# Performance work log

Measured on AMD Instinct MI355X. Metric: run time of the kernel, lower is better.

Reference implementation:

```python
import jax, jax.numpy as jnp
import numpy as np

B, L, C_IN = 16, 512, 32
D_MODEL, D_STATE, D_CONV, EXPAND, PRED_LEN = 128, 16, 4, 2, 96
D_INNER = EXPAND * D_MODEL          # 256
DT_RANK = (D_MODEL + 15) // 16      # 8 (ceil(d_model/16), mamba_ssm default)


def setup_inputs() -> dict:
    key = jax.random.key(0)
    ks = jax.random.split(key, 14)
    f32 = jnp.float32
    nrm = lambda k, shape, sc: jax.random.normal(k, shape, f32) * sc
    inp = {
        "x": jax.random.normal(ks[0], (B, L, C_IN), f32),
        # input_proj: Linear(enc_in, d_model)
        "W_in": nrm(ks[1], (C_IN, D_MODEL), C_IN ** -0.5),
        "b_in": jnp.zeros((D_MODEL,), f32),
        # Mamba in_proj: Linear(d_model, 2*d_inner, bias=False)
        "W_inproj": nrm(ks[2], (D_MODEL, 2 * D_INNER), D_MODEL ** -0.5),
        # depthwise causal conv1d (d_inner, d_conv) + bias
        "conv_w": nrm(ks[3], (D_INNER, D_CONV), D_CONV ** -0.5),
        "conv_b": jnp.zeros((D_INNER,), f32),
        # x_proj: Linear(d_inner, dt_rank + 2*d_state, bias=False)
        "W_xproj": nrm(ks[4], (D_INNER, DT_RANK + 2 * D_STATE), D_INNER ** -0.5),
        # dt_proj: Linear(dt_rank, d_inner) with bias init so softplus(bias) ~ 1e-3..1e-1
        "W_dt": nrm(ks[5], (DT_RANK, D_INNER), DT_RANK ** -0.5),
        "b_dt": jax.random.uniform(ks[6], (D_INNER,), f32, minval=-6.0, maxval=-3.0),
        # S4D-real A init: A = -exp(A_log), A_log = log(1..d_state)
        "A_log": jnp.log(jnp.tile(jnp.arange(1, D_STATE + 1, dtype=f32), (D_INNER, 1))),
        "D": jnp.ones((D_INNER,), f32),
        # Mamba out_proj: Linear(d_inner, d_model, bias=False)
        "W_out": nrm(ks[7], (D_INNER, D_MODEL), D_INNER ** -0.5),
        # output_proj: Linear(d_model*seq_len, pred_len*enc_in)
        "W_outproj": nrm(ks[8], (D_MODEL * L, PRED_LEN * C_IN), (D_MODEL * L) ** -0.5),
        "b_outproj": jnp.zeros((PRED_LEN * C_IN,), f32),
    }
    return inp


def _mamba_forward(x, W_in, b_in, W_inproj, conv_w, conv_b, W_xproj,
                   W_dt, b_dt, A_log, D, W_out, W_outproj, b_outproj):
    Bb, Ll, Cc = x.shape
    d_inner, d_conv = conv_w.shape
    d_state = A_log.shape[1]
    dt_rank = W_dt.shape[0]

    h = x @ W_in + b_in                                  # (B,L,d_model)
    xz = h @ W_inproj                                    # (B,L,2*d_inner)
    u, z = jnp.split(xz, 2, axis=-1)                     # each (B,L,d_inner)

    # causal depthwise conv1d along L
    uc = jnp.transpose(u, (0, 2, 1))                     # (B,d_inner,L)
    kern = conv_w[:, None, :]                            # (d_inner,1,d_conv)
    uc = jax.lax.conv_general_dilated(
        uc, kern, window_strides=(1,), padding=[(d_conv - 1, 0)],
        dimension_numbers=("NCH", "OIH", "NCH"), feature_group_count=d_inner)
    u = jax.nn.silu(jnp.transpose(uc, (0, 2, 1)) + conv_b)   # (B,L,d_inner)

    # input-dependent dt, B, C
    xdbc = u @ W_xproj                                   # (B,L,dt_rank+2*d_state)
    dt = jax.nn.softplus(xdbc[..., :dt_rank] @ W_dt + b_dt)  # (B,L,d_inner)
    Bm = xdbc[..., dt_rank:dt_rank + d_state]            # (B,L,d_state)
    Cm = xdbc[..., dt_rank + d_state:]                   # (B,L,d_state)

    A = -jnp.exp(A_log)                                  # (d_inner,d_state)
    dA = jnp.exp(jnp.einsum('bld,dn->bldn', dt, A))      # discretized A
    dBu = jnp.einsum('bld,bln,bld->bldn', dt, Bm, u)     # discretized B*u

    def step(hstate, inputs):
        dA_t, dBu_t, C_t = inputs                        # (B,d,n),(B,d,n),(B,n)
        hstate = dA_t * hstate + dBu_t
        y_t = jnp.einsum('bdn,bn->bd', hstate, C_t)
        return hstate, y_t

    h0 = jnp.zeros((Bb, d_inner, d_state), u.dtype)
    _, ys = jax.lax.scan(step, h0, (jnp.moveaxis(dA, 1, 0),
                                    jnp.moveaxis(dBu, 1, 0),
                                    jnp.moveaxis(Cm, 1, 0)))
    y = jnp.moveaxis(ys, 0, 1) + u * D                   # (B,L,d_inner)
    y = y * jax.nn.silu(z)                               # gating
    m_out = y @ W_out                                    # (B,L,d_model)

    flat = m_out.reshape(Bb, -1)                         # (B, L*d_model)
    pred = flat @ W_outproj + b_outproj                  # (B, pred_len*enc_in)
    return pred.reshape(Bb, W_outproj.shape[1] // Cc, Cc)


def reference(x, W_in, b_in, W_inproj, conv_w, conv_b, W_xproj,
              W_dt, b_dt, A_log, D, W_out, W_outproj, b_outproj):
    return _mamba_forward(x, W_in, b_in, W_inproj, conv_w, conv_b, W_xproj,
                          W_dt, b_dt, A_log, D, W_out, W_outproj, b_outproj)
```

## Files before the change

### kernel.cpp

```cpp
#include <hip/hip_runtime.h>
#include <math.h>

#define NB 16
#define LL 512
#define CIN 32
#define DM 128
#define DS 16
#define DI 256
#define DTR 8
#define NCOL 3072
#define KTOT 65536
#define ROWS 8192
#define CH 64
#define CLEN 8
#define KC 512
#define KS 128
#define OUTSZ 49152

typedef float f32x2 __attribute__((ext_vector_type(2)));

__device__ __forceinline__ float sigmoidf_(float x){ return 1.f/(1.f+expf(-x)); }
__device__ __forceinline__ float softplusf_(float x){ return (x > 20.f) ? x : log1pf(expf(x)); }

__global__ void __launch_bounds__(256) k_A(
    const float* __restrict__ x, const float* __restrict__ W_in,
    const float* __restrict__ b_in, const float* __restrict__ W_ip,
    const float* __restrict__ cw, const float* __restrict__ cb,
    float* __restrict__ u, float* __restrict__ z) {
  __shared__ float xs[11][32];
  __shared__ float hs[11][128];
  __shared__ float up[11][256];
  int t = threadIdx.x;
  int b  = blockIdx.x >> 6;
  int lt = blockIdx.x & 63;
  int l0 = lt * 8;
  for (int i=t; i<11*32; i+=256) {
    int r = i >> 5, c = i & 31;
    int li = l0 - 3 + r;
    xs[r][c] = (li >= 0) ? x[((b<<9)+li)*CIN + c] : 0.f;
  }
  __syncthreads();
  for (int i=t; i<11*128; i+=256) {
    int r = i >> 7, c = i & 127;
    float acc = b_in[c];
    #pragma unroll
    for (int k=0;k<CIN;k++) acc = fmaf(xs[r][k], W_in[k*DM+c], acc);
    hs[r][c] = acc;
  }
  __syncthreads();
  {
    int c0 = (t & 63)*4;
    int r0 = (t >> 6)*3;
    bool has2 = (r0+2 < 11);
    float acc[3][4] = {};
    for (int k4=0;k4<32;k4++) {
      float4 h0v = *(const float4*)&hs[r0][k4*4];
      float4 h1v = *(const float4*)&hs[r0+1][k4*4];
      float4 h2v = has2 ? *(const float4*)&hs[r0+2][k4*4] : make_float4(0.f,0.f,0.f,0.f);
      float h0a[4]={h0v.x,h0v.y,h0v.z,h0v.w};
      float h1a[4]={h1v.x,h1v.y,h1v.z,h1v.w};
      float h2a[4]={h2v.x,h2v.y,h2v.z,h2v.w};
      #pragma unroll
      for (int j=0;j<4;j++) {
        float4 w = *(const float4*)(W_ip + (k4*4+j)*512 + c0);
        acc[0][0]=fmaf(h0a[j],w.x,acc[0][0]); acc[0][1]=fmaf(h0a[j],w.y,acc[0][1]);
        acc[0][2]=fmaf(h0a[j],w.z,acc[0][2]); acc[0][3]=fmaf(h0a[j],w.w,acc[0][3]);
        acc[1][0]=fmaf(h1a[j],w.x,acc[1][0]); acc[1][1]=fmaf(h1a[j],w.y,acc[1][1]);
        acc[1][2]=fmaf(h1a[j],w.z,acc[1][2]); acc[1][3]=fmaf(h1a[j],w.w,acc[1][3]);
        acc[2][0]=fmaf(h2a[j],w.x,acc[2][0]); acc[2][1]=fmaf(h2a[j],w.y,acc[2][1]);
        acc[2][2]=fmaf(h2a[j],w.z,acc[2][2]); acc[2][3]=fmaf(h2a[j],w.w,acc[2][3]);
      }
    }
    *(float4*)&up[r0  ][c0] = make_float4(acc[0][0],acc[0][1],acc[0][2],acc[0][3]);
    *(float4*)&up[r0+1][c0] = make_float4(acc[1][0],acc[1][1],acc[1][2],acc[1][3]);
    if (has2)
      *(float4*)&up[r0+2][c0] = make_float4(acc[2][0],acc[2][1],acc[2][2],acc[2][3]);
  }
  {
    int c0 = (t & 63)*4;
    int r0 = (t >> 6)*2;
    float acc[2][4] = {};
    for (int k4=0;k4<32;k4++) {
      float4 h0v = *(const float4*)&hs[3+r0][k4*4];
      float4 h1v = *(const float4*)&hs[3+r0+1][k4*4];
      float h0a[4]={h0v.x,h0v.y,h0v.z,h0v.w};
      float h1a[4]={h1v.x,h1v.y,h1v.z,h1v.w};
      #pragma unroll
      for (int j=0;j<4;j++) {
        float4 w = *(const float4*)(W_ip + (k4*4+j)*512 + 256 + c0);
        acc[0][0]=fmaf(h0a[j],w.x,acc[0][0]); acc[0][1]=fmaf(h0a[j],w.y,acc[0][1]);
        acc[0][2]=fmaf(h0a[j],w.z,acc[0][2]); acc[0][3]=fmaf(h0a[j],w.w,acc[0][3]);
        acc[1][0]=fmaf(h1a[j],w.x,acc[1][0]); acc[1][1]=fmaf(h1a[j],w.y,acc[1][1]);
        acc[1][2]=fmaf(h1a[j],w.z,acc[1][2]); acc[1][3]=fmaf(h1a[j],w.w,acc[1][3]);
      }
    }
    #pragma unroll
    for (int i=0;i<2;i++) {
      int gr = (b<<9) + l0 + r0 + i;
      *(float4*)(z + gr*DI + c0) =
        make_float4(acc[i][0],acc[i][1],acc[i][2],acc[i][3]);
    }
  }
  __syncthreads();
  for (int i=t; i<8*256; i+=256) {
    int r = i >> 8, d = i & 255;
    float s = cb[d];
    #pragma unroll
    for (int j=0;j<4;j++) {
      int li = l0 + r - 3 + j;
      if (li >= 0) s = fmaf(cw[d*4+j], up[r+j][d], s);
    }
    int gr = (b<<9) + l0 + r;
    u[gr*DI + d] = s * sigmoidf_(s);
  }
}

__global__ void __launch_bounds__(256) k_xproj(
    const float* __restrict__ u, const float* __restrict__ W_xp,
    float* __restrict__ xdbc) {
  __shared__ float Wt[40][260];
  int t = threadIdx.x;
  for (int i=t; i<256*40; i+=256) {
    int k = i / 40, c = i - k*40;
    Wt[c][k] = W_xp[i];
  }
  __syncthreads();
  int idx = blockIdx.x*256 + t;
  int r = idx / 40, c = idx - r*40;
  const float4* ur4 = (const float4*)(u + r*DI);
  const float4* wc4 = (const float4*)&Wt[c][0];
  float acc = 0.f;
  #pragma unroll 8
  for (int k4=0;k4<64;k4++) {
    float4 uv = ur4[k4];
    float4 wv = wc4[k4];
    acc = fmaf(uv.x, wv.x, acc);
    acc = fmaf(uv.y, wv.y, acc);
    acc = fmaf(uv.z, wv.z, acc);
    acc = fmaf(uv.w, wv.w, acc);
  }
  xdbc[idx] = acc;
}

__global__ void __launch_bounds__(256) k_scan1(
    const float* __restrict__ u, const float* __restrict__ xdbc,
    const float* __restrict__ Wdt, const float* __restrict__ bdt,
    const float* __restrict__ A_log,
    float* __restrict__ Hc, float* __restrict__ Sdt) {
  __shared__ float xl[CLEN][40];
  int t = threadIdx.x;
  int b = blockIdx.x >> 6, c = blockIdx.x & 63, d = t;
  int l0 = c * CLEN;
  int row0 = (b<<9) + l0;
  for (int i=t; i<CLEN*40; i+=256) xl[i/40][i%40] = xdbc[row0*40 + i];
  __syncthreads();
  float A[16], hsv[16];
  #pragma unroll
  for (int n=0;n<16;n++){ A[n] = -expf(A_log[d*16+n]); hsv[n]=0.f; }
  float wdt[DTR];
  #pragma unroll
  for (int j=0;j<DTR;j++) wdt[j] = Wdt[j*DI+d];
  float bdtv = bdt[d];
  float sdt = 0.f;
  for (int l=0;l<CLEN;++l) {
    float acc = bdtv;
    #pragma unroll
    for (int j=0;j<DTR;j++) acc = fmaf(xl[l][j], wdt[j], acc);
    float dtv = softplusf_(acc);
    sdt += dtv;
    float du = dtv * u[((row0+l)<<8) + d];
    #pragma unroll
    for (int n=0;n<16;n++) {
      float a = expf(dtv*A[n]);
      hsv[n] = fmaf(a, hsv[n], du * xl[l][DTR+n]);
    }
  }
  int bd = (b<<8) + d;
  int base = (bd*CH + c)*16;
  #pragma unroll
  for (int n=0;n<16;n++) Hc[base+n] = hsv[n];
  Sdt[bd*CH + c] = sdt;
}

__global__ void k_scan2(const float* __restrict__ A_log, const float* __restrict__ Hc,
                        const float* __restrict__ Sdt, float* __restrict__ Hst) {
  int idx = blockIdx.x*256 + threadIdx.x;
  int n  = idx & 15;
  int bd = idx >> 4;
  int d  = bd & 255;
  float A = -expf(A_log[d*16+n]);
  float hs = 0.f;
  int base = bd*CH*16;
  for (int c=0;c<CH;c++) {
    Hst[base + c*16 + n] = hs;
    float sdt = Sdt[bd*CH + c];
    hs = fmaf(expf(A*sdt), hs, Hc[base + c*16 + n]);
  }
}

__global__ void __launch_bounds__(256) k_scan3(
    const float* __restrict__ u, const float* __restrict__ z,
    const float* __restrict__ xdbc, const float* __restrict__ Wdt,
    const float* __restrict__ bdt, const float* __restrict__ A_log,
    const float* __restrict__ Dp, const float* __restrict__ Hst,
    const float* __restrict__ W_out, float* __restrict__ mo) {
  __shared__ float ym[CLEN][256];
  __shared__ float xl[CLEN][40];
  int t = threadIdx.x;
  int b = blockIdx.x >> 6, c = blockIdx.x & 63, d = t;
  int l0 = c * CLEN;
  int row0 = (b<<9) + l0;
  for (int i=t; i<CLEN*40; i+=256) xl[i/40][i%40] = xdbc[row0*40 + i];
  __syncthreads();
  int bd = (b<<8) + d;
  int base = (bd*CH + c)*16;
  float A[16], hsv[16];
  #pragma unroll
  for (int n=0;n<16;n++){ A[n] = -expf(A_log[d*16+n]); hsv[n] = Hst[base+n]; }
  float wdt[DTR];
  #pragma unroll
  for (int j=0;j<DTR;j++) wdt[j] = Wdt[j*DI+d];
  float bdtv = bdt[d];
  float Dv = Dp[d];
  for (int l=0;l<CLEN;++l) {
    int row = row0 + l;
    float acc = bdtv;
    #pragma unroll
    for (int j=0;j<DTR;j++) acc = fmaf(xl[l][j], wdt[j], acc);
    float dtv = softplusf_(acc);
    float uv = u[(row<<8) + d];
    float zv = z[(row<<8) + d];
    float du = dtv * uv;
    float y = 0.f;
    #pragma unroll
    for (int n=0;n<16;n++) {
      float a = expf(dtv*A[n]);
      hsv[n] = fmaf(a, hsv[n], du * xl[l][DTR+n]);
      y = fmaf(hsv[n], xl[l][DTR+DS+n], y);
    }
    y = fmaf(uv, Dv, y);
    ym[l][d] = y * (zv * sigmoidf_(zv));
  }
  __syncthreads();
  int cc = t & 127;
  int rg = (t >> 7) * 4;
  float acc[4] = {};
  for (int k4=0;k4<64;k4++) {
    float w0 = W_out[(k4*4+0)*DM+cc];
    float w1 = W_out[(k4*4+1)*DM+cc];
    float w2 = W_out[(k4*4+2)*DM+cc];
    float w3 = W_out[(k4*4+3)*DM+cc];
    #pragma unroll
    for (int o=0;o<4;o++) {
      float4 yv = *(const float4*)&ym[rg+o][k4*4];
      acc[o] = fmaf(yv.w, w3, fmaf(yv.z, w2, fmaf(yv.y, w1, fmaf(yv.x, w0, acc[o]))));
    }
  }
  #pragma unroll
  for (int o=0;o<4;o++) mo[(row0+rg+o)*DM + cc] = acc[o];
}

__global__ void __launch_bounds__(256) k_final(
    const float* __restrict__ flat, const float* __restrict__ W,
    float* __restrict__ part) {
  __shared__ float lds[KC][16];
  int t = threadIdx.x;
  int n0 = blockIdx.x * 512;
  int k0 = blockIdx.y * KC;
  for (int i = t; i < 16*(KC/4); i += 256) {
    int bb  = i & 15;
    int kk4 = i >> 4;
    float4 v = *(const float4*)(flat + bb*KTOT + k0 + kk4*4);
    lds[kk4*4+0][bb] = v.x; lds[kk4*4+1][bb] = v.y;
    lds[kk4*4+2][bb] = v.z; lds[kk4*4+3][bb] = v.w;
  }
  __syncthreads();
  int c0 = n0 + t*2;
  float2 acc[16];
  #pragma unroll
  for (int b=0;b<16;b++) acc[b] = make_float2(0.f,0.f);
  const float* Wp = W + (size_t)k0*NCOL + c0;
  for (int kk=0; kk<KC; kk+=4) {
    f32x2 w0 = __builtin_nontemporal_load((const f32x2*)(Wp + (size_t)(kk+0)*NCOL));
    f32x2 w1 = __builtin_nontemporal_load((const f32x2*)(Wp + (size_t)(kk+1)*NCOL));
    f32x2 w2 = __builtin_nontemporal_load((const f32x2*)(Wp + (size_t)(kk+2)*NCOL));
    f32x2 w3 = __builtin_nontemporal_load((const f32x2*)(Wp + (size_t)(kk+3)*NCOL));
    const float4* f0 = (const float4*)&lds[kk+0][0];
    const float4* f1 = (const float4*)&lds[kk+1][0];
    const float4* f2 = (const float4*)&lds[kk+2][0];
    const float4* f3 = (const float4*)&lds[kk+3][0];
    #pragma unroll
    for (int q=0;q<4;q++) {
      float4 fa = f0[q], fb = f1[q], fc = f2[q], fd = f3[q];
      float fs0[4] = {fa.x,fa.y,fa.z,fa.w};
      float fs1[4] = {fb.x,fb.y,fb.z,fb.w};
      float fs2[4] = {fc.x,fc.y,fc.z,fc.w};
      float fs3[4] = {fd.x,fd.y,fd.z,fd.w};
      #pragma unroll
      for (int j=0;j<4;j++) {
        int b = q*4+j;
        acc[b].x=fmaf(fs0[j],w0.x,acc[b].x); acc[b].y=fmaf(fs0[j],w0.y,acc[b].y);
        acc[b].x=fmaf(fs1[j],w1.x,acc[b].x); acc[b].y=fmaf(fs1[j],w1.y,acc[b].y);
        acc[b].x=fmaf(fs2[j],w2.x,acc[b].x); acc[b].y=fmaf(fs2[j],w2.y,acc[b].y);
        acc[b].x=fmaf(fs3[j],w3.x,acc[b].x); acc[b].y=fmaf(fs3[j],w3.y,acc[b].y);
      }
    }
  }
  float* p = part + (size_t)blockIdx.y*OUTSZ;
  #pragma unroll
  for (int b=0;b<16;b++) {
    f32x2 v; v.x = acc[b].x; v.y = acc[b].y;
    __builtin_nontemporal_store(v, (f32x2*)(p + b*NCOL + c0));
  }
}

__global__ void k_reduce(const float* __restrict__ part, const float* __restrict__ bias,
                         float* __restrict__ out) {
  int idx = blockIdx.x*256 + threadIdx.x;
  float acc = bias[idx % NCOL];
  #pragma unroll 8
  for (int s=0;s<KS;s++)
    acc += __builtin_nontemporal_load(part + (size_t)s*OUTSZ + idx);
  out[idx] = acc;
}

extern "C" void kernel_launch(void* const* d_in, const int* in_sizes, int n_in,
                              void* d_out, int out_size, void* d_ws, size_t ws_size,
                              hipStream_t stream) {
  const float* x        = (const float*)d_in[0];
  const float* W_in     = (const float*)d_in[1];
  const float* b_in     = (const float*)d_in[2];
  const float* W_inproj = (const float*)d_in[3];
  const float* conv_w   = (const float*)d_in[4];
  const float* conv_b   = (const float*)d_in[5];
  const float* W_xproj  = (const float*)d_in[6];
  const float* W_dt     = (const float*)d_in[7];
  const float* b_dt     = (const float*)d_in[8];
  const float* A_log    = (const float*)d_in[9];
  const float* Dp       = (const float*)d_in[10];
  const float* W_out    = (const float*)d_in[11];
  const float* W_outproj= (const float*)d_in[12];
  const float* b_outproj= (const float*)d_in[13];
  float* out = (float*)d_out;
  float* ws  = (float*)d_ws;

  float* u    = ws;
  float* z    = ws + 2097152;
  float* xdbc = ws + 4194304;
  float* Hc   = ws + 4521984;
  float* Sdt  = ws + 8716288;
  float* Hst  = ws + 8978432;
  float* mo   = ws + 13172736;
  float* part = ws + 14221312;

  k_A     <<<1024, 256, 0, stream>>>(x, W_in, b_in, W_inproj, conv_w, conv_b, u, z);
  k_xproj <<<1280, 256, 0, stream>>>(u, W_xproj, xdbc);
  k_scan1 <<<1024, 256, 0, stream>>>(u, xdbc, W_dt, b_dt, A_log, Hc, Sdt);
  k_scan2 <<<256,  256, 0, stream>>>(A_log, Hc, Sdt, Hst);
  k_scan3 <<<1024, 256, 0, stream>>>(u, z, xdbc, W_dt, b_dt, A_log, Dp, Hst, W_out, mo);
  k_final <<<dim3(6, KS), 256, 0, stream>>>(mo, W_outproj, part);
  k_reduce<<<192,  256, 0, stream>>>(part, b_outproj, out);
}
```

Measured before the change: 290.4 us.

## Merge five pre-projection kernels into one cooperative kernel with grid syncs

Replaces the separate input-projection, x_proj, chunk-scan, chunk-carry and output-scan kernels with a single cooperative kernel of 512 blocks. The stages are separated by grid.sync(), and each block loops over two work units per stage. This removes four kernel launch boundaries. The x_proj stage also drops its LDS-transposed weight staging and reads W_xproj directly from global memory. In exchange, the kernel has higher LDS usage, half-idle grid phases (the carry stage uses only 256 blocks), grid-barrier costs, and uncoalesced weight reads in x_proj.

```diff
diff --git a/kernel.cpp b/kernel.cpp
--- a/kernel.cpp
+++ b/kernel.cpp
@@ -1,5 +1,8 @@
 #include <hip/hip_runtime.h>
+#include <hip/hip_cooperative_groups.h>
 #include <math.h>
+
+namespace cg = cooperative_groups;
 
 #define NB 16
 #define LL 512
@@ -16,248 +19,243 @@
 #define KC 512
 #define KS 128
 #define OUTSZ 49152
+#define MGRID 512
 
 typedef float f32x2 __attribute__((ext_vector_type(2)));
 
 __device__ __forceinline__ float sigmoidf_(float x){ return 1.f/(1.f+expf(-x)); }
 __device__ __forceinline__ float softplusf_(float x){ return (x > 20.f) ? x : log1pf(expf(x)); }
 
-__global__ void __launch_bounds__(256) k_A(
+__global__ void __launch_bounds__(256) k_mega(
     const float* __restrict__ x, const float* __restrict__ W_in,
     const float* __restrict__ b_in, const float* __restrict__ W_ip,
     const float* __restrict__ cw, const float* __restrict__ cb,
-    float* __restrict__ u, float* __restrict__ z) {
+    const float* __restrict__ W_xp, const float* __restrict__ Wdt,
+    const float* __restrict__ bdt, const float* __restrict__ A_log,
+    const float* __restrict__ Dp, const float* __restrict__ W_out,
+    float* __restrict__ u, float* __restrict__ z,
+    float* __restrict__ xdbc, float* __restrict__ Hc,
+    float* __restrict__ Sdt, float* __restrict__ Hst,
+    float* __restrict__ mo) {
+  cg::grid_group grid = cg::this_grid();
   __shared__ float xs[11][32];
   __shared__ float hs[11][128];
   __shared__ float up[11][256];
+  __shared__ float xl[CLEN][40];
+  __shared__ float ym[CLEN][256];
   int t = threadIdx.x;
-  int b  = blockIdx.x >> 6;
-  int lt = blockIdx.x & 63;
-  int l0 = lt * 8;
-  for (int i=t; i<11*32; i+=256) {
-    int r = i >> 5, c = i & 31;
-    int li = l0 - 3 + r;
-    xs[r][c] = (li >= 0) ? x[((b<<9)+li)*CIN + c] : 0.f;
-  }
-  __syncthreads();
-  for (int i=t; i<11*128; i+=256) {
-    int r = i >> 7, c = i & 127;
-    float acc = b_in[c];
-    #pragma unroll
-    for (int k=0;k<CIN;k++) acc = fmaf(xs[r][k], W_in[k*DM+c], acc);
-    hs[r][c] = acc;
-  }
-  __syncthreads();
-  {
-    int c0 = (t & 63)*4;
-    int r0 = (t >> 6)*3;
-    bool has2 = (r0+2 < 11);
-    float acc[3][4] = {};
-    for (int k4=0;k4<32;k4++) {
-      float4 h0v = *(const float4*)&hs[r0][k4*4];
-      float4 h1v = *(const float4*)&hs[r0+1][k4*4];
-      float4 h2v = has2 ? *(const float4*)&hs[r0+2][k4*4] : make_float4(0.f,0.f,0.f,0.f);
-      float h0a[4]={h0v.x,h0v.y,h0v.z,h0v.w};
-      float h1a[4]={h1v.x,h1v.y,h1v.z,h1v.w};
-      float h2a[4]={h2v.x,h2v.y,h2v.z,h2v.w};
+
+  for (int rep=0; rep<2; ++rep) {
+    int unit = blockIdx.x + (rep<<9);
+    int b = unit >> 6;
+    int l0 = (unit & 63) * 8;
+    for (int i=t; i<11*32; i+=256) {
+      int r = i >> 5, c = i & 31;
+      int li = l0 - 3 + r;
+      xs[r][c] = (li >= 0) ? x[((b<<9)+li)*CIN + c] : 0.f;
+    }
+    __syncthreads();
+    for (int i=t; i<11*128; i+=256) {
+      int r = i >> 7, c = i & 127;
+      float acc = b_in[c];
+      #pragma unroll
+      for (int k=0;k<CIN;k++) acc = fmaf(xs[r][k], W_in[k*DM+c], acc);
+      hs[r][c] = acc;
+    }
+    __syncthreads();
+    {
+      int c0 = (t & 63)*4;
+      int r0 = (t >> 6)*3;
+      bool has2 = (r0+2 < 11);
+      float acc[3][4] = {};
+      for (int k4=0;k4<32;k4++) {
+        float4 h0v = *(const float4*)&hs[r0][k4*4];
+        float4 h1v = *(const float4*)&hs[r0+1][k4*4];
+        float4 h2v = has2 ? *(const float4*)&hs[r0+2][k4*4] : make_float4(0.f,0.f,0.f,0.f);
+        float h0a[4]={h0v.x,h0v.y,h0v.z,h0v.w};
+        float h1a[4]={h1v.x,h1v.y,h1v.z,h1v.w};
+        float h2a[4]={h2v.x,h2v.y,h2v.z,h2v.w};
+        #pragma unroll
+        for (int j=0;j<4;j++) {
+          float4 w = *(const float4*)(W_ip + (k4*4+j)*512 + c0);
+          acc[0][0]=fmaf(h0a[j],w.x,acc[0][0]); acc[0][1]=fmaf(h0a[j],w.y,acc[0][1]);
+          acc[0][2]=fmaf(h0a[j],w.z,acc[0][2]); acc[0][3]=fmaf(h0a[j],w.w,acc[0][3]);
+          acc[1][0]=fmaf(h1a[j],w.x,acc[1][0]); acc[1][1]=fmaf(h1a[j],w.y,acc[1][1]);
+          acc[1][2]=fmaf(h1a[j],w.z,acc[1][2]); acc[1][3]=fmaf(h1a[j],w.w,acc[1][3]);
+          acc[2][0]=fmaf(h2a[j],w.x,acc[2][0]); acc[2][1]=fmaf(h2a[j],w.y,acc[2][1]);
+          acc[2][2]=fmaf(h2a[j],w.z,acc[2][2]); acc[2][3]=fmaf(h2a[j],w.w,acc[2][3]);
+        }
+      }
+      *(float4*)&up[r0  ][c0] = make_float4(acc[0][0],acc[0][1],acc[0][2],acc[0][3]);
+      *(float4*)&up[r0+1][c0] = make_float4(acc[1][0],acc[1][1],acc[1][2],acc[1][3]);
+      if (has2)
+        *(float4*)&up[r0+2][c0] = make_float4(acc[2][0],acc[2][1],acc[2][2],acc[2][3]);
+    }
+    {
+      int c0 = (t & 63)*4;
+      int r0 = (t >> 6)*2;
+      float acc[2][4] = {};
+      for (int k4=0;k4<32;k4++) {
+        float4 h0v = *(const float4*)&hs[3+r0][k4*4];
+        float4 h1v = *(const float4*)&hs[3+r0+1][k4*4];
+        float h0a[4]={h0v.x,h0v.y,h0v.z,h0v.w};
+        float h1a[4]={h1v.x,h1v.y,h1v.z,h1v.w};
+        #pragma unroll
+        for (int j=0;j<4;j++) {
+          float4 w = *(const float4*)(W_ip + (k4*4+j)*512 + 256 + c0);
+          acc[0][0]=fmaf(h0a[j],w.x,acc[0][0]); acc[0][1]=fmaf(h0a[j],w.y,acc[0][1]);
+          acc[0][2]=fmaf(h0a[j],w.z,acc[0][2]); acc[0][3]=fmaf(h0a[j],w.w,acc[0][3]);
+          acc[1][0]=fmaf(h1a[j],w.x,acc[1][0]); acc[1][1]=fmaf(h1a[j],w.y,acc[1][1]);
+          acc[1][2]=fmaf(h1a[j],w.z,acc[1][2]); acc[1][3]=fmaf(h1a[j],w.w,acc[1][3]);
+        }
+      }
+      #pragma unroll
+      for (int i=0;i<2;i++) {
+        int gr = (b<<9) + l0 + r0 + i;
+        *(float4*)(z + gr*DI + c0) =
+          make_float4(acc[i][0],acc[i][1],acc[i][2],acc[i][3]);
+      }
+    }
+    __syncthreads();
+    for (int i=t; i<8*256; i+=256) {
+      int r = i >> 8, d = i & 255;
+      float s = cb[d];
       #pragma unroll
       for (int j=0;j<4;j++) {
-        float4 w = *(const float4*)(W_ip + (k4*4+j)*512 + c0);
-        acc[0][0]=fmaf(h0a[j],w.x,acc[0][0]); acc[0][1]=fmaf(h0a[j],w.y,acc[0][1]);
-        acc[0][2]=fmaf(h0a[j],w.z,acc[0][2]); acc[0][3]=fmaf(h0a[j],w.w,acc[0][3]);
-        acc[1][0]=fmaf(h1a[j],w.x,acc[1][0]); acc[1][1]=fmaf(h1a[j],w.y,acc[1][1]);
-        acc[1][2]=fmaf(h1a[j],w.z,acc[1][2]); acc[1][3]=fmaf(h1a[j],w.w,acc[1][3]);
-        acc[2][0]=fmaf(h2a[j],w.x,acc[2][0]); acc[2][1]=fmaf(h2a[j],w.y,acc[2][1]);
-        acc[2][2]=fmaf(h2a[j],w.z,acc[2][2]); acc[2][3]=fmaf(h2a[j],w.w,acc[2][3]);
-      }
-    }
-    *(float4*)&up[r0  ][c0] = make_float4(acc[0][0],acc[0][1],acc[0][2],acc[0][3]);
-    *(float4*)&up[r0+1][c0] = make_float4(acc[1][0],acc[1][1],acc[1][2],acc[1][3]);
-    if (has2)
-      *(float4*)&up[r0+2][c0] = make_float4(acc[2][0],acc[2][1],acc[2][2],acc[2][3]);
-  }
-  {
-    int c0 = (t & 63)*4;
-    int r0 = (t >> 6)*2;
-    float acc[2][4] = {};
-    for (int k4=0;k4<32;k4++) {
-      float4 h0v = *(const float4*)&hs[3+r0][k4*4];
-      float4 h1v = *(const float4*)&hs[3+r0+1][k4*4];
-      float h0a[4]={h0v.x,h0v.y,h0v.z,h0v.w};
-      float h1a[4]={h1v.x,h1v.y,h1v.z,h1v.w};
-      #pragma unroll
-      for (int j=0;j<4;j++) {
-        float4 w = *(const float4*)(W_ip + (k4*4+j)*512 + 256 + c0);
-        acc[0][0]=fmaf(h0a[j],w.x,acc[0][0]); acc[0][1]=fmaf(h0a[j],w.y,acc[0][1]);
-        acc[0][2]=fmaf(h0a[j],w.z,acc[0][2]); acc[0][3]=fmaf(h0a[j],w.w,acc[0][3]);
-        acc[1][0]=fmaf(h1a[j],w.x,acc[1][0]); acc[1][1]=fmaf(h1a[j],w.y,acc[1][1]);
-        acc[1][2]=fmaf(h1a[j],w.z,acc[1][2]); acc[1][3]=fmaf(h1a[j],w.w,acc[1][3]);
-      }
-    }
-    #pragma unroll
-    for (int i=0;i<2;i++) {
-      int gr = (b<<9) + l0 + r0 + i;
-      *(float4*)(z + gr*DI + c0) =
-        make_float4(acc[i][0],acc[i][1],acc[i][2],acc[i][3]);
-    }
-  }
-  __syncthreads();
-  for (int i=t; i<8*256; i+=256) {
-    int r = i >> 8, d = i & 255;
-    float s = cb[d];
-    #pragma unroll
-    for (int j=0;j<4;j++) {
-      int li = l0 + r - 3 + j;
-      if (li >= 0) s = fmaf(cw[d*4+j], up[r+j][d], s);
-    }
-    int gr = (b<<9) + l0 + r;
-    u[gr*DI + d] = s * sigmoidf_(s);
-  }
-}
-
-__global__ void __launch_bounds__(256) k_xproj(
-    const float* __restrict__ u, const float* __restrict__ W_xp,
-    float* __restrict__ xdbc) {
-  __shared__ float Wt[40][260];
-  int t = threadIdx.x;
-  for (int i=t; i<256*40; i+=256) {
-    int k = i / 40, c = i - k*40;
-    Wt[c][k] = W_xp[i];
-  }
-  __syncthreads();
-  int idx = blockIdx.x*256 + t;
-  int r = idx / 40, c = idx - r*40;
-  const float4* ur4 = (const float4*)(u + r*DI);
-  const float4* wc4 = (const float4*)&Wt[c][0];
-  float acc = 0.f;
-  #pragma unroll 8
-  for (int k4=0;k4<64;k4++) {
-    float4 uv = ur4[k4];
-    float4 wv = wc4[k4];
-    acc = fmaf(uv.x, wv.x, acc);
-    acc = fmaf(uv.y, wv.y, acc);
-    acc = fmaf(uv.z, wv.z, acc);
-    acc = fmaf(uv.w, wv.w, acc);
-  }
-  xdbc[idx] = acc;
-}
-
-__global__ void __launch_bounds__(256) k_scan1(
-    const float* __restrict__ u, const float* __restrict__ xdbc,
-    const float* __restrict__ Wdt, const float* __restrict__ bdt,
-    const float* __restrict__ A_log,
-    float* __restrict__ Hc, float* __restrict__ Sdt) {
-  __shared__ float xl[CLEN][40];
-  int t = threadIdx.x;
-  int b = blockIdx.x >> 6, c = blockIdx.x & 63, d = t;
-  int l0 = c * CLEN;
-  int row0 = (b<<9) + l0;
-  for (int i=t; i<CLEN*40; i+=256) xl[i/40][i%40] = xdbc[row0*40 + i];
-  __syncthreads();
-  float A[16], hsv[16];
-  #pragma unroll
-  for (int n=0;n<16;n++){ A[n] = -expf(A_log[d*16+n]); hsv[n]=0.f; }
-  float wdt[DTR];
-  #pragma unroll
-  for (int j=0;j<DTR;j++) wdt[j] = Wdt[j*DI+d];
-  float bdtv = bdt[d];
-  float sdt = 0.f;
-  for (int l=0;l<CLEN;++l) {
-    float acc = bdtv;
-    #pragma unroll
-    for (int j=0;j<DTR;j++) acc = fmaf(xl[l][j], wdt[j], acc);
-    float dtv = softplusf_(acc);
-    sdt += dtv;
-    float du = dtv * u[((row0+l)<<8) + d];
-    #pragma unroll
-    for (int n=0;n<16;n++) {
-      float a = expf(dtv*A[n]);
-      hsv[n] = fmaf(a, hsv[n], du * xl[l][DTR+n]);
-    }
-  }
-  int bd = (b<<8) + d;
-  int base = (bd*CH + c)*16;
-  #pragma unroll
-  for (int n=0;n<16;n++) Hc[base+n] = hsv[n];
-  Sdt[bd*CH + c] = sdt;
-}
-
-__global__ void k_scan2(const float* __restrict__ A_log, const float* __restrict__ Hc,
-                        const float* __restrict__ Sdt, float* __restrict__ Hst) {
-  int idx = blockIdx.x*256 + threadIdx.x;
-  int n  = idx & 15;
-  int bd = idx >> 4;
-  int d  = bd & 255;
-  float A = -expf(A_log[d*16+n]);
-  float hs = 0.f;
-  int base = bd*CH*16;
-  for (int c=0;c<CH;c++) {
-    Hst[base + c*16 + n] = hs;
-    float sdt = Sdt[bd*CH + c];
-    hs = fmaf(expf(A*sdt), hs, Hc[base + c*16 + n]);
-  }
-}
-
-__global__ void __launch_bounds__(256) k_scan3(
-    const float* __restrict__ u, const float* __restrict__ z,
-    const float* __restrict__ xdbc, const float* __restrict__ Wdt,
-    const float* __restrict__ bdt, const float* __restrict__ A_log,
-    const float* __restrict__ Dp, const float* __restrict__ Hst,
-    const float* __restrict__ W_out, float* __restrict__ mo) {
-  __shared__ float ym[CLEN][256];
-  __shared__ float xl[CLEN][40];
-  int t = threadIdx.x;
-  int b = blockIdx.x >> 6, c = blockIdx.x & 63, d = t;
-  int l0 = c * CLEN;
-  int row0 = (b<<9) + l0;
-  for (int i=t; i<CLEN*40; i+=256) xl[i/40][i%40] = xdbc[row0*40 + i];
-  __syncthreads();
-  int bd = (b<<8) + d;
-  int base = (bd*CH + c)*16;
-  float A[16], hsv[16];
-  #pragma unroll
-  for (int n=0;n<16;n++){ A[n] = -expf(A_log[d*16+n]); hsv[n] = Hst[base+n]; }
-  float wdt[DTR];
-  #pragma unroll
-  for (int j=0;j<DTR;j++) wdt[j] = Wdt[j*DI+d];
-  float bdtv = bdt[d];
-  float Dv = Dp[d];
-  for (int l=0;l<CLEN;++l) {
-    int row = row0 + l;
-    float acc = bdtv;
-    #pragma unroll
-    for (int j=0;j<DTR;j++) acc = fmaf(xl[l][j], wdt[j], acc);
-    float dtv = softplusf_(acc);
-    float uv = u[(row<<8) + d];
-    float zv = z[(row<<8) + d];
-    float du = dtv * uv;
-    float y = 0.f;
-    #pragma unroll
-    for (int n=0;n<16;n++) {
-      float a = expf(dtv*A[n]);
-      hsv[n] = fmaf(a, hsv[n], du * xl[l][DTR+n]);
-      y = fmaf(hsv[n], xl[l][DTR+DS+n], y);
-    }
-    y = fmaf(uv, Dv, y);
-    ym[l][d] = y * (zv * sigmoidf_(zv));
-  }
-  __syncthreads();
-  int cc = t & 127;
-  int rg = (t >> 7) * 4;
-  float acc[4] = {};
-  for (int k4=0;k4<64;k4++) {
-    float w0 = W_out[(k4*4+0)*DM+cc];
-    float w1 = W_out[(k4*4+1)*DM+cc];
-    float w2 = W_out[(k4*4+2)*DM+cc];
-    float w3 = W_out[(k4*4+3)*DM+cc];
-    #pragma unroll
-    for (int o=0;o<4;o++) {
-      float4 yv = *(const float4*)&ym[rg+o][k4*4];
-      acc[o] = fmaf(yv.w, w3, fmaf(yv.z, w2, fmaf(yv.y, w1, fmaf(yv.x, w0, acc[o]))));
-    }
-  }
-  #pragma unroll
-  for (int o=0;o<4;o++) mo[(row0+rg+o)*DM + cc] = acc[o];
+        int li = l0 + r - 3 + j;
+        if (li >= 0) s = fmaf(cw[d*4+j], up[r+j][d], s);
+      }
+      int gr = (b<<9) + l0 + r;
+      u[gr*DI + d] = s * sigmoidf_(s);
+    }
+    __syncthreads();
+  }
+  grid.sync();
+
+  for (int idx = blockIdx.x*256 + t; idx < ROWS*40; idx += MGRID*256) {
+    int r = idx / 40, c = idx - r*40;
+    const float4* ur4 = (const float4*)(u + r*DI);
+    float acc = 0.f;
+    #pragma unroll 8
+    for (int k4=0;k4<64;k4++) {
+      float4 uv = ur4[k4];
+      acc = fmaf(uv.x, W_xp[(k4*4+0)*40+c], acc);
+      acc = fmaf(uv.y, W_xp[(k4*4+1)*40+c], acc);
+      acc = fmaf(uv.z, W_xp[(k4*4+2)*40+c], acc);
+      acc = fmaf(uv.w, W_xp[(k4*4+3)*40+c], acc);
+    }
+    xdbc[idx] = acc;
+  }
+  grid.sync();
+
+  for (int rep=0; rep<2; ++rep) {
+    int unit = blockIdx.x + (rep<<9);
+    int b = unit >> 6, c = unit & 63, d = t;
+    int l0 = c * CLEN;
+    int row0 = (b<<9) + l0;
+    for (int i=t; i<CLEN*40; i+=256) xl[i/40][i%40] = xdbc[row0*40 + i];
+    __syncthreads();
+    float A[16], hsv[16];
+    #pragma unroll
+    for (int n=0;n<16;n++){ A[n] = -expf(A_log[d*16+n]); hsv[n]=0.f; }
+    float wdt[DTR];
+    #pragma unroll
+    for (int j=0;j<DTR;j++) wdt[j] = Wdt[j*DI+d];
+    float bdtv = bdt[d];
+    float sdt = 0.f;
+    for (int l=0;l<CLEN;++l) {
+      float acc = bdtv;
+      #pragma unroll
+      for (int j=0;j<DTR;j++) acc = fmaf(xl[l][j], wdt[j], acc);
+      float dtv = softplusf_(acc);
+      sdt += dtv;
+      float du = dtv * u[((row0+l)<<8) + d];
+      #pragma unroll
+      for (int n=0;n<16;n++) {
+        float a = expf(dtv*A[n]);
+        hsv[n] = fmaf(a, hsv[n], du * xl[l][DTR+n]);
+      }
+    }
+    int bd = (b<<8) + d;
+    int base = (bd*CH + c)*16;
+    #pragma unroll
+    for (int n=0;n<16;n++) Hc[base+n] = hsv[n];
+    Sdt[bd*CH + c] = sdt;
+    __syncthreads();
+  }
+  grid.sync();
+
+  if (blockIdx.x < 256) {
+    int idx = blockIdx.x*256 + t;
+    int n  = idx & 15;
+    int bd = idx >> 4;
+    int d  = bd & 255;
+    float A = -expf(A_log[d*16+n]);
+    float hsl = 0.f;
+    int base = bd*CH*16;
+    for (int c=0;c<CH;c++) {
+      Hst[base + c*16 + n] = hsl;
+      float sdt = Sdt[bd*CH + c];
+      hsl = fmaf(expf(A*sdt), hsl, Hc[base + c*16 + n]);
+    }
+  }
+  grid.sync();
+
+  for (int rep=0; rep<2; ++rep) {
+    int unit = blockIdx.x + (rep<<9);
+    int b = unit >> 6, c = unit & 63, d = t;
+    int l0 = c * CLEN;
+    int row0 = (b<<9) + l0;
+    for (int i=t; i<CLEN*40; i+=256) xl[i/40][i%40] = xdbc[row0*40 + i];
+    __syncthreads();
+    int bd = (b<<8) + d;
+    int base = (bd*CH + c)*16;
+    float A[16], hsv[16];
+    #pragma unroll
+    for (int n=0;n<16;n++){ A[n] = -expf(A_log[d*16+n]); hsv[n] = Hst[base+n]; }
+    float wdt[DTR];
+    #pragma unroll
+    for (int j=0;j<DTR;j++) wdt[j] = Wdt[j*DI+d];
+    float bdtv = bdt[d];
+    float Dv = Dp[d];
+    for (int l=0;l<CLEN;++l) {
+      int row = row0 + l;
+      float acc = bdtv;
+      #pragma unroll
+      for (int j=0;j<DTR;j++) acc = fmaf(xl[l][j], wdt[j], acc);
+      float dtv = softplusf_(acc);
+      float uv = u[(row<<8) + d];
+      float zv = z[(row<<8) + d];
+      float du = dtv * uv;
+      float y = 0.f;
+      #pragma unroll
+      for (int n=0;n<16;n++) {
+        float a = expf(dtv*A[n]);
+        hsv[n] = fmaf(a, hsv[n], du * xl[l][DTR+n]);
+        y = fmaf(hsv[n], xl[l][DTR+DS+n], y);
+      }
+      y = fmaf(uv, Dv, y);
+      ym[l][d] = y * (zv * sigmoidf_(zv));
+    }
+    __syncthreads();
+    int cc = t & 127;
+    int rg = (t >> 7) * 4;
+    float acc[4] = {};
+    for (int k4=0;k4<64;k4++) {
+      float w0 = W_out[(k4*4+0)*DM+cc];
+      float w1 = W_out[(k4*4+1)*DM+cc];
+      float w2 = W_out[(k4*4+2)*DM+cc];
+      float w3 = W_out[(k4*4+3)*DM+cc];
+      #pragma unroll
+      for (int o=0;o<4;o++) {
+        float4 yv = *(const float4*)&ym[rg+o][k4*4];
+        acc[o] = fmaf(yv.w, w3, fmaf(yv.z, w2, fmaf(yv.y, w1, fmaf(yv.x, w0, acc[o]))));
+      }
+    }
+    #pragma unroll
+    for (int o=0;o<4;o++) mo[(row0+rg+o)*DM + cc] = acc[o];
+    __syncthreads();
+  }
 }
 
 __global__ void __launch_bounds__(256) k_final(
@@ -353,11 +351,14 @@
   float* mo   = ws + 13172736;
   float* part = ws + 14221312;
 
-  k_A     <<<1024, 256, 0, stream>>>(x, W_in, b_in, W_inproj, conv_w, conv_b, u, z);
-  k_xproj <<<1280, 256, 0, stream>>>(u, W_xproj, xdbc);
-  k_scan1 <<<1024, 256, 0, stream>>>(u, xdbc, W_dt, b_dt, A_log, Hc, Sdt);
-  k_scan2 <<<256,  256, 0, stream>>>(A_log, Hc, Sdt, Hst);
-  k_scan3 <<<1024, 256, 0, stream>>>(u, z, xdbc, W_dt, b_dt, A_log, Dp, Hst, W_out, mo);
+  void* args[] = {
+    (void*)&x, (void*)&W_in, (void*)&b_in, (void*)&W_inproj,
+    (void*)&conv_w, (void*)&conv_b, (void*)&W_xproj, (void*)&W_dt,
+    (void*)&b_dt, (void*)&A_log, (void*)&Dp, (void*)&W_out,
+    (void*)&u, (void*)&z, (void*)&xdbc, (void*)&Hc,
+    (void*)&Sdt, (void*)&Hst, (void*)&mo
+  };
+  hipLaunchCooperativeKernel((void*)k_mega, dim3(MGRID), dim3(256), args, 0, stream);
   k_final <<<dim3(6, KS), 256, 0, stream>>>(mo, W_outproj, part);
   k_reduce<<<192,  256, 0, stream>>>(part, b_outproj, out);
 }
```

After: 553.7 us. +90.7%, slower.
